# Optimization experiments

Hardware: AMD Instinct MI355X
Metric: run time of the kernel (lower is better)

Reference implementation:

```python
import jax, jax.numpy as jnp
import numpy as np
import math

B = 16384
INPUT = 2048
HIDDEN = 2048
PROJ = 1024


def setup_inputs() -> dict:
    key = jax.random.key(0)
    ks = jax.random.split(key, 20)
    stdv = 1.0 / math.sqrt(PROJ)
    u = lambda k, shape: jax.random.uniform(k, shape, jnp.float32, -stdv, stdv)
    return {
        "x_t": jax.random.normal(ks[0], (B, INPUT), jnp.float32),
        "h_t": jax.random.normal(ks[1], (B, PROJ), jnp.float32),
        "c_t": jax.random.normal(ks[2], (B, HIDDEN), jnp.float32),
        "weight_if_x": u(ks[3], (INPUT, 2 * HIDDEN)),
        "weight_if_h": u(ks[4], (PROJ, 2 * HIDDEN)),
        "weight_if_c": u(ks[5], (HIDDEN, 2 * HIDDEN)),
        "bias_i": u(ks[6], (HIDDEN,)),
        "bias_f": u(ks[7], (HIDDEN,)),
        "weight_c_x": u(ks[8], (INPUT, HIDDEN)),
        "weight_c_h": u(ks[9], (PROJ, HIDDEN)),
        "bias_c": u(ks[10], (HIDDEN,)),
        "weight_o_x": u(ks[11], (INPUT, PROJ)),
        "weight_o_h": u(ks[12], (PROJ, PROJ)),
        "weight_o_c": u(ks[13], (HIDDEN, PROJ)),
        "bias_o": u(ks[14], (PROJ,)),
        "weight_r_proj": u(ks[15], (HIDDEN, PROJ)),
        "weight_r_x": u(ks[16], (INPUT, PROJ)),
    }


def reference(x_t, h_t, c_t, weight_if_x, weight_if_h, weight_if_c, bias_i, bias_f,
              weight_c_x, weight_c_h, bias_c, weight_o_x, weight_o_h, weight_o_c,
              bias_o, weight_r_proj, weight_r_x):
    # input/forget gates with peephole on c_t: [B, 2*HIDDEN]
    if_gates = x_t @ weight_if_x + h_t @ weight_if_h + c_t @ weight_if_c
    ingate, forgetgate = jnp.split(if_gates, 2, axis=-1)
    ingate = jax.nn.sigmoid(ingate + bias_i)
    forgetgate = jax.nn.sigmoid(forgetgate + bias_f)
    cellgate = jnp.tanh(x_t @ weight_c_x + h_t @ weight_c_h + bias_c)
    c_new = forgetgate * c_t + ingate * cellgate
    # output gate peeps at new cell state
    outgate = jax.nn.sigmoid(x_t @ weight_o_x + h_t @ weight_o_h + c_new @ weight_o_c + bias_o)
    r_t = jnp.tanh(c_new)
    m_t = r_t @ weight_r_proj
    # input_size != proj_size -> project x for the residual connection
    h_new = outgate * (m_t + x_t @ weight_r_x)
    return (h_new, c_new)
```

## Files before the change

kernel.cpp:

```cpp
#include <hip/hip_runtime.h>
#include <hip/hip_bf16.h>
#include <math.h>

typedef unsigned short u16;
typedef __bf16 bf16x8_t __attribute__((ext_vector_type(8)));
typedef float  f32x4_t  __attribute__((ext_vector_type(4)));
typedef float  f32x8_t  __attribute__((ext_vector_type(8)));
typedef u16    u16x4_t  __attribute__((ext_vector_type(4)));
typedef u16    u16x8_t  __attribute__((ext_vector_type(8)));

__device__ __forceinline__ u16 f2b(float f) {
  unsigned u = __builtin_bit_cast(unsigned, f);
  u += 0x7fffu + ((u >> 16) & 1u);
  return (u16)(u >> 16);
}
__device__ __forceinline__ float b2f(u16 h) {
  unsigned u = ((unsigned)h) << 16;
  return __builtin_bit_cast(float, u);
}
__device__ __forceinline__ float sigm_(float x) { return 1.0f / (1.0f + __expf(-x)); }
__device__ __forceinline__ float tanh_(float x) { return 1.0f - 2.0f / (__expf(2.0f * x) + 1.0f); }

__device__ __forceinline__ void gload16(const void* g, void* l) {
  __builtin_amdgcn_global_load_lds(
      (__attribute__((address_space(1))) void*)(g),
      (__attribute__((address_space(3))) void*)(l), 16, 0, 0);
}


__global__ void cvt_act_kernel(const float* __restrict__ src, u16* __restrict__ dst,
                               int C, int KT, int c0) {
  int mb = blockIdx.x, ktl = blockIdx.y, t = threadIdx.x;
  int ktg = (c0 >> 5) + ktl;
  const float* s = src + (long)(mb * 256 + t) * C + ktl * 32;
  u16* d = dst + ((long)(mb * KT + ktg)) * 8192 + t * 8;
#pragma unroll
  for (int p = 0; p < 4; ++p) {
    f32x8_t v = *(const f32x8_t*)(s + p * 8);
    u16x8_t o;
#pragma unroll
    for (int r = 0; r < 8; ++r) o[r] = f2b(v[r]);
    *(u16x8_t*)(d + p * 2048) = o;
  }
}

__global__ void cvt_wt_kernel(const float* __restrict__ src, u16* __restrict__ dst,
                              int N, int KT, int n0, int k0) {
  int bx = blockIdx.x, by = blockIdx.y, t = threadIdx.x;
  int n = bx * 256 + t;
  int nb_g = (n0 >> 8) + bx;
  int ktg = (k0 >> 5) + by;
  float tmp[32];
#pragma unroll
  for (int kk = 0; kk < 32; ++kk)
    tmp[kk] = src[(long)(by * 32 + kk) * N + n];
  u16* d = dst + ((long)(nb_g * KT + ktg)) * 8192 + t * 8;
#pragma unroll
  for (int p = 0; p < 4; ++p) {
    u16x8_t o;
#pragma unroll
    for (int r = 0; r < 8; ++r) o[r] = f2b(tmp[p * 8 + r]);
    *(u16x8_t*)(d + p * 2048) = o;
  }
}

template <int MODE>
__global__ __launch_bounds__(512, 2) void gemm256_kernel(
    const u16* __restrict__ A, const u16* __restrict__ Bt, u16* __restrict__ Cout) {
  constexpr int KT   = (MODE == 0) ? 160 : 128;
  constexpr int NCOL = (MODE == 0) ? 8192 : 2048;
  constexpr int NBN  = NCOL / 256;
  constexpr int SLOT = 16384;

  __shared__ u16 lds[3 * SLOT];

  int bid = blockIdx.x;
  int cpx = gridDim.x >> 3;
  bid = (bid & 7) * cpx + (bid >> 3);

  int mb = bid / NBN, nb = bid % NBN;
  int m0 = mb * 256, n0 = nb * 256;

  int kt0, NT;
  if (MODE == 0) { kt0 = 0; NT = (nb < 16) ? 160 : ((nb < 28) ? 96 : 64); }
  else           { kt0 = (nb < 4) ? 0 : 64; NT = 64; }

  const int tid  = threadIdx.x;
  const int lane = tid & 63;
  const int wid  = tid >> 6;
  const int wr   = wid >> 2;
  const int wc   = wid & 3;

  const int segoff = wid * 512 + lane * 8;
  const u16* baseA = A  + ((long)(mb * KT + kt0)) * 8192 + segoff;
  const u16* baseB = Bt + ((long)(nb * KT + kt0)) * 8192 + segoff;

#define STAGE_A(t, s) do { \
    gload16(baseA + (long)(t) * 8192,        &lds[(s) * SLOT + segoff]); \
    gload16(baseA + (long)(t) * 8192 + 4096, &lds[(s) * SLOT + segoff + 4096]); } while (0)
#define STAGE_B(t, s) do { \
    gload16(baseB + (long)(t) * 8192,        &lds[(s) * SLOT + 8192 + segoff]); \
    gload16(baseB + (long)(t) * 8192 + 4096, &lds[(s) * SLOT + 8192 + segoff + 4096]); } while (0)

  const int aoff = (lane >> 4) * 2048 + (wr * 128 + (lane & 15)) * 8;
  const int boff = (lane >> 4) * 2048 + (wc * 64  + (lane & 15)) * 8;

  f32x4_t acc[8][4];
#pragma unroll
  for (int m = 0; m < 8; ++m)
#pragma unroll
    for (int n = 0; n < 4; ++n) acc[m][n] = (f32x4_t){0.f, 0.f, 0.f, 0.f};

  STAGE_A(0, 0); STAGE_B(0, 0);
  STAGE_A(1, 1); STAGE_B(1, 1);
  asm volatile("s_waitcnt vmcnt(4)" ::: "memory");
  __builtin_amdgcn_s_barrier();

  int slot = 0, s2 = 2;
  for (int t = 0; t < NT; ++t) {
    const u16* sA = &lds[slot * SLOT];
    const u16* sB = sA + 8192;
    const bool pre = (t + 2 < NT);

    if (pre) { STAGE_A(t + 2, s2); STAGE_B(t + 2, s2); }

    bf16x8_t bv[4], av[8];
#pragma unroll
    for (int n = 0; n < 4; ++n) bv[n] = *(const bf16x8_t*)&sB[boff + n * 128];
#pragma unroll
    for (int m = 0; m < 8; ++m) av[m] = *(const bf16x8_t*)&sA[aoff + m * 128];

    __builtin_amdgcn_s_setprio(1);
#pragma unroll
    for (int m = 0; m < 8; ++m)
#pragma unroll
      for (int n = 0; n < 4; ++n)
        acc[m][n] = __builtin_amdgcn_mfma_f32_16x16x32_bf16(bv[n], av[m], acc[m][n], 0, 0, 0);
    __builtin_amdgcn_s_setprio(0);

    if (pre) asm volatile("s_waitcnt vmcnt(4)" ::: "memory");
    else     asm volatile("s_waitcnt vmcnt(0)" ::: "memory");
    __builtin_amdgcn_s_barrier();

    slot = (slot == 2) ? 0 : slot + 1;
    s2   = (s2   == 2) ? 0 : s2   + 1;
  }
#undef STAGE_A
#undef STAGE_B

  const int rowm = lane & 15;
  const int col4 = (lane >> 4) * 4;
#pragma unroll
  for (int m = 0; m < 8; ++m) {
    long rg = (long)(m0 + wr * 128 + m * 16 + rowm) * NCOL;
#pragma unroll
    for (int n = 0; n < 4; ++n) {
      int cg = n0 + wc * 64 + n * 16 + col4;
      u16x4_t o;
#pragma unroll
      for (int r = 0; r < 4; ++r) o[r] = f2b(acc[m][n][r]);
      *(u16x4_t*)&Cout[rg + cg] = o;
    }
  }
}

__global__ void pass2_kernel(const u16* __restrict__ G1, const float* __restrict__ c_t,
                             const float* __restrict__ bias_i, const float* __restrict__ bias_f,
                             const float* __restrict__ bias_c,
                             float* __restrict__ c_new_out, u16* __restrict__ A2p) {
  int mb = blockIdx.x, jg = blockIdx.y, t = threadIdx.x;
  int b = mb * 256 + t;
  int j0 = jg * 32;
  const u16* row = G1 + (long)b * 8192 + j0;
  const float* cp_p = c_t + (long)b * 2048 + j0;
  float* co_p = c_new_out + (long)b * 2048 + j0;
  u16* dc = A2p + ((long)(mb * 128 + jg)) * 8192 + t * 8;
  u16* dr = dc + (long)64 * 8192;

#pragma unroll
  for (int q = 0; q < 4; ++q) {
    u16x8_t ip = *(const u16x8_t*)(row + q * 8);
    u16x8_t fp = *(const u16x8_t*)(row + 2048 + q * 8);
    u16x8_t gp = *(const u16x8_t*)(row + 4096 + q * 8);
    f32x8_t cp = *(const f32x8_t*)(cp_p + q * 8);
    f32x8_t bi = *(const f32x8_t*)(bias_i + j0 + q * 8);
    f32x8_t bf = *(const f32x8_t*)(bias_f + j0 + q * 8);
    f32x8_t bc = *(const f32x8_t*)(bias_c + j0 + q * 8);
    f32x8_t cn;
    u16x8_t cb, rb;
#pragma unroll
    for (int r = 0; r < 8; ++r) {
      float ig = sigm_(b2f(ip[r]) + bi[r]);
      float fg = sigm_(b2f(fp[r]) + bf[r]);
      float g  = tanh_(b2f(gp[r]) + bc[r]);
      float c  = fg * cp[r] + ig * g;
      cn[r] = c;
      cb[r] = f2b(c);
      rb[r] = f2b(tanh_(c));
    }
    *(f32x8_t*)(co_p + q * 8) = cn;
    *(u16x8_t*)(dc + q * 2048) = cb;
    *(u16x8_t*)(dr + q * 2048) = rb;
  }
}

__global__ void pass3_kernel(const u16* __restrict__ G1, const u16* __restrict__ G2,
                             const float* __restrict__ bias_o, float* __restrict__ h_out) {
  long i = (long)blockIdx.x * blockDim.x + threadIdx.x;
  long e = i * 8;
  int b = (int)(e >> 10);
  int j = (int)(e & 1023);
  const u16* row1 = G1 + (long)b * 8192;
  const u16* row2 = G2 + (long)b * 2048;
  u16x8_t ogp = *(const u16x8_t*)(row1 + 6144 + j);
  u16x8_t xrp = *(const u16x8_t*)(row1 + 7168 + j);
  u16x8_t ocg = *(const u16x8_t*)(row2 + j);
  u16x8_t mt  = *(const u16x8_t*)(row2 + 1024 + j);
  f32x8_t bo  = *(const f32x8_t*)(bias_o + j);
  f32x8_t h;
#pragma unroll
  for (int r = 0; r < 8; ++r) {
    float og = sigm_(b2f(ogp[r]) + b2f(ocg[r]) + bo[r]);
    h[r] = og * (b2f(mt[r]) + b2f(xrp[r]));
  }
  *(f32x8_t*)(h_out + (long)b * 1024 + j) = h;
}

extern "C" void kernel_launch(void* const* d_in, const int* in_sizes, int n_in,
                              void* d_out, int out_size, void* d_ws, size_t ws_size,
                              hipStream_t stream) {
  const float* x_t      = (const float*)d_in[0];
  const float* h_t      = (const float*)d_in[1];
  const float* c_t      = (const float*)d_in[2];
  const float* w_if_x   = (const float*)d_in[3];
  const float* w_if_h   = (const float*)d_in[4];
  const float* w_if_c   = (const float*)d_in[5];
  const float* bias_i   = (const float*)d_in[6];
  const float* bias_f   = (const float*)d_in[7];
  const float* w_c_x    = (const float*)d_in[8];
  const float* w_c_h    = (const float*)d_in[9];
  const float* bias_c   = (const float*)d_in[10];
  const float* w_o_x    = (const float*)d_in[11];
  const float* w_o_h    = (const float*)d_in[12];
  const float* w_o_c    = (const float*)d_in[13];
  const float* bias_o   = (const float*)d_in[14];
  const float* w_r_proj = (const float*)d_in[15];
  const float* w_r_x    = (const float*)d_in[16];

  char* ws = (char*)d_ws;
  u16* A1p  = (u16*)(ws);
  u16* W1tp = (u16*)(ws + 167772160L);
  u16* G1   = (u16*)(ws + 251658240L);
  u16* W2tp = (u16*)(ws + 520093696L);
  u16* A2p  = (u16*)(ws);
  u16* G2   = (u16*)(ws + 167772160L);

  float* h_out = (float*)d_out;
  float* c_out = h_out + 16384L * 1024L;

  cvt_act_kernel<<<dim3(64, 64), 256, 0, stream>>>(x_t, A1p, 2048, 160, 0);
  cvt_act_kernel<<<dim3(64, 32), 256, 0, stream>>>(h_t, A1p, 1024, 160, 2048);
  cvt_act_kernel<<<dim3(64, 64), 256, 0, stream>>>(c_t, A1p, 2048, 160, 3072);

  cvt_wt_kernel<<<dim3(16, 64), 256, 0, stream>>>(w_if_x,   W1tp, 4096, 160, 0,    0);
  cvt_wt_kernel<<<dim3(16, 32), 256, 0, stream>>>(w_if_h,   W1tp, 4096, 160, 0,    2048);
  cvt_wt_kernel<<<dim3(16, 64), 256, 0, stream>>>(w_if_c,   W1tp, 4096, 160, 0,    3072);
  cvt_wt_kernel<<<dim3(8,  64), 256, 0, stream>>>(w_c_x,    W1tp, 2048, 160, 4096, 0);
  cvt_wt_kernel<<<dim3(8,  32), 256, 0, stream>>>(w_c_h,    W1tp, 2048, 160, 4096, 2048);
  cvt_wt_kernel<<<dim3(4,  64), 256, 0, stream>>>(w_o_x,    W1tp, 1024, 160, 6144, 0);
  cvt_wt_kernel<<<dim3(4,  32), 256, 0, stream>>>(w_o_h,    W1tp, 1024, 160, 6144, 2048);
  cvt_wt_kernel<<<dim3(4,  64), 256, 0, stream>>>(w_r_x,    W1tp, 1024, 160, 7168, 0);
  cvt_wt_kernel<<<dim3(4,  64), 256, 0, stream>>>(w_o_c,    W2tp, 1024, 128, 0,    0);
  cvt_wt_kernel<<<dim3(4,  64), 256, 0, stream>>>(w_r_proj, W2tp, 1024, 128, 1024, 2048);

  gemm256_kernel<0><<<2048, 512, 0, stream>>>(A1p, W1tp, G1);

  pass2_kernel<<<dim3(64, 64), 256, 0, stream>>>(G1, c_t, bias_i, bias_f, bias_c, c_out, A2p);

  gemm256_kernel<1><<<512, 512, 0, stream>>>(A2p, W2tp, G2);

  pass3_kernel<<<8192, 256, 0, stream>>>(G1, G2, bias_o, h_out);
}
```

Before: 1.501 ms.

## Switch GEMM to 32x32x16 MFMA tiles and merge conversion launches

The GEMM inner loop now uses 32x32x16 bf16 MFMA with 16-wide accumulators instead of 16x16x32, which halves the LDS fragment reads per FLOP and issues fewer MFMA instructions. The LDS read pattern and the epilogue store mapping change to match the new output layout. The thirteen separate activation and weight conversion launches are also merged into three kernels that pick their source by block index, cutting launch overhead. The larger MFMA tile may change register pressure and LDS bank-conflict behaviour.

```diff
diff --git a/kernel.cpp b/kernel.cpp
--- a/kernel.cpp
+++ b/kernel.cpp
@@ -4,8 +4,8 @@
 
 typedef unsigned short u16;
 typedef __bf16 bf16x8_t __attribute__((ext_vector_type(8)));
-typedef float  f32x4_t  __attribute__((ext_vector_type(4)));
 typedef float  f32x8_t  __attribute__((ext_vector_type(8)));
+typedef float  f32x16_t __attribute__((ext_vector_type(16)));
 typedef u16    u16x4_t  __attribute__((ext_vector_type(4)));
 typedef u16    u16x8_t  __attribute__((ext_vector_type(8)));
 
@@ -28,12 +28,15 @@
 }
 
 
-__global__ void cvt_act_kernel(const float* __restrict__ src, u16* __restrict__ dst,
-                               int C, int KT, int c0) {
-  int mb = blockIdx.x, ktl = blockIdx.y, t = threadIdx.x;
-  int ktg = (c0 >> 5) + ktl;
-  const float* s = src + (long)(mb * 256 + t) * C + ktl * 32;
-  u16* d = dst + ((long)(mb * KT + ktg)) * 8192 + t * 8;
+__global__ void pack_act_kernel(const float* __restrict__ x, const float* __restrict__ h,
+                                const float* __restrict__ c, u16* __restrict__ A1p) {
+  int mb = blockIdx.x, kt = blockIdx.y, t = threadIdx.x;
+  const float* src; int C, ccol;
+  if (kt < 64)      { src = x; C = 2048; ccol = kt * 32; }
+  else if (kt < 96) { src = h; C = 1024; ccol = (kt - 64) * 32; }
+  else              { src = c; C = 2048; ccol = (kt - 96) * 32; }
+  const float* s = src + (long)(mb * 256 + t) * C + ccol;
+  u16* d = A1p + ((long)(mb * 160 + kt)) * 8192 + t * 8;
 #pragma unroll
   for (int p = 0; p < 4; ++p) {
     f32x8_t v = *(const f32x8_t*)(s + p * 8);
@@ -44,17 +47,61 @@
   }
 }
 
-__global__ void cvt_wt_kernel(const float* __restrict__ src, u16* __restrict__ dst,
-                              int N, int KT, int n0, int k0) {
-  int bx = blockIdx.x, by = blockIdx.y, t = threadIdx.x;
-  int n = bx * 256 + t;
-  int nb_g = (n0 >> 8) + bx;
-  int ktg = (k0 >> 5) + by;
+__global__ void pack_w1_kernel(const float* __restrict__ w_if_x, const float* __restrict__ w_if_h,
+                               const float* __restrict__ w_if_c, const float* __restrict__ w_c_x,
+                               const float* __restrict__ w_c_h,  const float* __restrict__ w_o_x,
+                               const float* __restrict__ w_o_h,  const float* __restrict__ w_r_x,
+                               u16* __restrict__ W1tp) {
+  int nb = blockIdx.x, kt = blockIdx.y, t = threadIdx.x;
+  int n0g = nb * 256;
+  const float* src; int N, nl, kl;
+  if (n0g < 4096) {
+    N = 4096; nl = n0g;
+    if (kt < 64)      { src = w_if_x; kl = kt * 32; }
+    else if (kt < 96) { src = w_if_h; kl = (kt - 64) * 32; }
+    else              { src = w_if_c; kl = (kt - 96) * 32; }
+  } else if (n0g < 6144) {
+    N = 2048; nl = n0g - 4096;
+    if (kt < 64)      { src = w_c_x; kl = kt * 32; }
+    else if (kt < 96) { src = w_c_h; kl = (kt - 64) * 32; }
+    else return;
+  } else if (n0g < 7168) {
+    N = 1024; nl = n0g - 6144;
+    if (kt < 64)      { src = w_o_x; kl = kt * 32; }
+    else if (kt < 96) { src = w_o_h; kl = (kt - 64) * 32; }
+    else return;
+  } else {
+    N = 1024; nl = n0g - 7168;
+    if (kt < 64)      { src = w_r_x; kl = kt * 32; }
+    else return;
+  }
+  int n = nl + t;
   float tmp[32];
 #pragma unroll
   for (int kk = 0; kk < 32; ++kk)
-    tmp[kk] = src[(long)(by * 32 + kk) * N + n];
-  u16* d = dst + ((long)(nb_g * KT + ktg)) * 8192 + t * 8;
+    tmp[kk] = src[(long)(kl + kk) * N + n];
+  u16* d = W1tp + ((long)(nb * 160 + kt)) * 8192 + t * 8;
+#pragma unroll
+  for (int p = 0; p < 4; ++p) {
+    u16x8_t o;
+#pragma unroll
+    for (int r = 0; r < 8; ++r) o[r] = f2b(tmp[p * 8 + r]);
+    *(u16x8_t*)(d + p * 2048) = o;
+  }
+}
+
+__global__ void pack_w2_kernel(const float* __restrict__ w_o_c,
+                               const float* __restrict__ w_r_proj, u16* __restrict__ W2tp) {
+  int nb = blockIdx.x, kt = blockIdx.y, t = threadIdx.x;
+  const float* src; int nl, kl;
+  if (nb < 4) { if (kt >= 64) return; src = w_o_c;    nl = nb * 256;       kl = kt * 32; }
+  else        { if (kt < 64)  return; src = w_r_proj; nl = (nb - 4) * 256; kl = (kt - 64) * 32; }
+  int n = nl + t;
+  float tmp[32];
+#pragma unroll
+  for (int kk = 0; kk < 32; ++kk)
+    tmp[kk] = src[(long)(kl + kk) * 1024 + n];
+  u16* d = W2tp + ((long)(nb * 128 + kt)) * 8192 + t * 8;
 #pragma unroll
   for (int p = 0; p < 4; ++p) {
     u16x8_t o;
@@ -67,7 +114,7 @@
 template <int MODE>
 __global__ __launch_bounds__(512, 2) void gemm256_kernel(
     const u16* __restrict__ A, const u16* __restrict__ Bt, u16* __restrict__ Cout) {
-  constexpr int KT   = (MODE == 0) ? 160 : 128;
+  constexpr int KTF  = (MODE == 0) ? 160 : 128;
   constexpr int NCOL = (MODE == 0) ? 8192 : 2048;
   constexpr int NBN  = NCOL / 256;
   constexpr int SLOT = 16384;
@@ -90,29 +137,31 @@
   const int wid  = tid >> 6;
   const int wr   = wid >> 2;
   const int wc   = wid & 3;
-
-  const int segoff = wid * 512 + lane * 8;
-  const u16* baseA = A  + ((long)(mb * KT + kt0)) * 8192 + segoff;
-  const u16* baseB = Bt + ((long)(nb * KT + kt0)) * 8192 + segoff;
-
-#define STAGE_A(t, s) do { \
-    gload16(baseA + (long)(t) * 8192,        &lds[(s) * SLOT + segoff]); \
-    gload16(baseA + (long)(t) * 8192 + 4096, &lds[(s) * SLOT + segoff + 4096]); } while (0)
-#define STAGE_B(t, s) do { \
-    gload16(baseB + (long)(t) * 8192,        &lds[(s) * SLOT + 8192 + segoff]); \
-    gload16(baseB + (long)(t) * 8192 + 4096, &lds[(s) * SLOT + 8192 + segoff + 4096]); } while (0)
-
-  const int aoff = (lane >> 4) * 2048 + (wr * 128 + (lane & 15)) * 8;
-  const int boff = (lane >> 4) * 2048 + (wc * 64  + (lane & 15)) * 8;
-
-  f32x4_t acc[8][4];
-#pragma unroll
-  for (int m = 0; m < 8; ++m)
-#pragma unroll
-    for (int n = 0; n < 4; ++n) acc[m][n] = (f32x4_t){0.f, 0.f, 0.f, 0.f};
-
-  STAGE_A(0, 0); STAGE_B(0, 0);
-  STAGE_A(1, 1); STAGE_B(1, 1);
+  const int l31  = lane & 31;
+  const int hl   = lane >> 5;
+
+  const int dstg = tid * 8;
+  const u16* pA = A  + ((long)(mb * KTF + kt0)) * 8192 + dstg;
+  const u16* pB = Bt + ((long)(nb * KTF + kt0)) * 8192 + dstg;
+
+#define STAGE(t, s) do { \
+    gload16(pA + (long)(t) * 8192,        &lds[(s) * SLOT + dstg]); \
+    gload16(pA + (long)(t) * 8192 + 4096, &lds[(s) * SLOT + dstg + 4096]); \
+    gload16(pB + (long)(t) * 8192,        &lds[(s) * SLOT + 8192 + dstg]); \
+    gload16(pB + (long)(t) * 8192 + 4096, &lds[(s) * SLOT + 8192 + dstg + 4096]); } while (0)
+
+  const int abase = (wr * 128 + l31) * 8;
+  const int bbase = (wc * 64  + l31) * 8;
+
+  f32x16_t acc[4][2];
+#pragma unroll
+  for (int m = 0; m < 4; ++m)
+#pragma unroll
+    for (int n = 0; n < 2; ++n)
+#pragma unroll
+      for (int r = 0; r < 16; ++r) acc[m][n][r] = 0.f;
+
+  STAGE(0, 0); STAGE(1, 1);
   asm volatile("s_waitcnt vmcnt(4)" ::: "memory");
   __builtin_amdgcn_s_barrier();
 
@@ -121,21 +170,31 @@
     const u16* sA = &lds[slot * SLOT];
     const u16* sB = sA + 8192;
     const bool pre = (t + 2 < NT);
-
-    if (pre) { STAGE_A(t + 2, s2); STAGE_B(t + 2, s2); }
-
-    bf16x8_t bv[4], av[8];
-#pragma unroll
-    for (int n = 0; n < 4; ++n) bv[n] = *(const bf16x8_t*)&sB[boff + n * 128];
-#pragma unroll
-    for (int m = 0; m < 8; ++m) av[m] = *(const bf16x8_t*)&sA[aoff + m * 128];
+    if (pre) STAGE(t + 2, s2);
+
+    bf16x8_t xa[4], xb[4], wa[2], wb[2];
+#pragma unroll
+    for (int m = 0; m < 4; ++m) {
+      xa[m] = *(const bf16x8_t*)&sA[hl * 2048 + abase + m * 256];
+      xb[m] = *(const bf16x8_t*)&sA[(2 + hl) * 2048 + abase + m * 256];
+    }
+#pragma unroll
+    for (int n = 0; n < 2; ++n) {
+      wa[n] = *(const bf16x8_t*)&sB[hl * 2048 + bbase + n * 256];
+      wb[n] = *(const bf16x8_t*)&sB[(2 + hl) * 2048 + bbase + n * 256];
+    }
 
     __builtin_amdgcn_s_setprio(1);
 #pragma unroll
-    for (int m = 0; m < 8; ++m)
-#pragma unroll
-      for (int n = 0; n < 4; ++n)
-        acc[m][n] = __builtin_amdgcn_mfma_f32_16x16x32_bf16(bv[n], av[m], acc[m][n], 0, 0, 0);
+    for (int m = 0; m < 4; ++m)
+#pragma unroll
+      for (int n = 0; n < 2; ++n)
+        acc[m][n] = __builtin_amdgcn_mfma_f32_32x32x16_bf16(wa[n], xa[m], acc[m][n], 0, 0, 0);
+#pragma unroll
+    for (int m = 0; m < 4; ++m)
+#pragma unroll
+      for (int n = 0; n < 2; ++n)
+        acc[m][n] = __builtin_amdgcn_mfma_f32_32x32x16_bf16(wb[n], xb[m], acc[m][n], 0, 0, 0);
     __builtin_amdgcn_s_setprio(0);
 
     if (pre) asm volatile("s_waitcnt vmcnt(4)" ::: "memory");
@@ -145,21 +204,22 @@
     slot = (slot == 2) ? 0 : slot + 1;
     s2   = (s2   == 2) ? 0 : s2   + 1;
   }
-#undef STAGE_A
-#undef STAGE_B
-
-  const int rowm = lane & 15;
-  const int col4 = (lane >> 4) * 4;
-#pragma unroll
-  for (int m = 0; m < 8; ++m) {
-    long rg = (long)(m0 + wr * 128 + m * 16 + rowm) * NCOL;
-#pragma unroll
-    for (int n = 0; n < 4; ++n) {
-      int cg = n0 + wc * 64 + n * 16 + col4;
-      u16x4_t o;
-#pragma unroll
-      for (int r = 0; r < 4; ++r) o[r] = f2b(acc[m][n][r]);
-      *(u16x4_t*)&Cout[rg + cg] = o;
+#undef STAGE
+
+  const long rowg = (long)(m0 + wr * 128 + l31);
+  const int  colg = n0 + wc * 64 + 4 * hl;
+#pragma unroll
+  for (int mm = 0; mm < 4; ++mm) {
+    long rb = (rowg + mm * 32) * (long)NCOL;
+#pragma unroll
+    for (int nn = 0; nn < 2; ++nn) {
+#pragma unroll
+      for (int g = 0; g < 4; ++g) {
+        u16x4_t o;
+#pragma unroll
+        for (int r = 0; r < 4; ++r) o[r] = f2b(acc[mm][nn][g * 4 + r]);
+        *(u16x4_t*)&Cout[rb + colg + nn * 32 + g * 8] = o;
+      }
     }
   }
 }
@@ -258,20 +318,10 @@
   float* h_out = (float*)d_out;
   float* c_out = h_out + 16384L * 1024L;
 
-  cvt_act_kernel<<<dim3(64, 64), 256, 0, stream>>>(x_t, A1p, 2048, 160, 0);
-  cvt_act_kernel<<<dim3(64, 32), 256, 0, stream>>>(h_t, A1p, 1024, 160, 2048);
-  cvt_act_kernel<<<dim3(64, 64), 256, 0, stream>>>(c_t, A1p, 2048, 160, 3072);
-
-  cvt_wt_kernel<<<dim3(16, 64), 256, 0, stream>>>(w_if_x,   W1tp, 4096, 160, 0,    0);
-  cvt_wt_kernel<<<dim3(16, 32), 256, 0, stream>>>(w_if_h,   W1tp, 4096, 160, 0,    2048);
-  cvt_wt_kernel<<<dim3(16, 64), 256, 0, stream>>>(w_if_c,   W1tp, 4096, 160, 0,    3072);
-  cvt_wt_kernel<<<dim3(8,  64), 256, 0, stream>>>(w_c_x,    W1tp, 2048, 160, 4096, 0);
-  cvt_wt_kernel<<<dim3(8,  32), 256, 0, stream>>>(w_c_h,    W1tp, 2048, 160, 4096, 2048);
-  cvt_wt_kernel<<<dim3(4,  64), 256, 0, stream>>>(w_o_x,    W1tp, 1024, 160, 6144, 0);
-  cvt_wt_kernel<<<dim3(4,  32), 256, 0, stream>>>(w_o_h,    W1tp, 1024, 160, 6144, 2048);
-  cvt_wt_kernel<<<dim3(4,  64), 256, 0, stream>>>(w_r_x,    W1tp, 1024, 160, 7168, 0);
-  cvt_wt_kernel<<<dim3(4,  64), 256, 0, stream>>>(w_o_c,    W2tp, 1024, 128, 0,    0);
-  cvt_wt_kernel<<<dim3(4,  64), 256, 0, stream>>>(w_r_proj, W2tp, 1024, 128, 1024, 2048);
+  pack_act_kernel<<<dim3(64, 160), 256, 0, stream>>>(x_t, h_t, c_t, A1p);
+  pack_w1_kernel<<<dim3(32, 160), 256, 0, stream>>>(w_if_x, w_if_h, w_if_c, w_c_x, w_c_h,
+                                                    w_o_x, w_o_h, w_r_x, W1tp);
+  pack_w2_kernel<<<dim3(8, 128), 256, 0, stream>>>(w_o_c, w_r_proj, W2tp);
 
   gemm256_kernel<0><<<2048, 512, 0, stream>>>(A1p, W1tp, G1);
 
```

New measurement: 1.569 ms. 1.05x slower.
